# Kernel tuning notes

Measured on AMD Instinct MI355X. Metric: run time of the kernel, lower is better.

Reference implementation:

```python
import jax, jax.numpy as jnp
import numpy as np
import math

B, H, S, D = 4, 8, 2048, 64

def setup_inputs() -> dict:
    key = jax.random.key(0)
    k1, k2, k3, k4 = jax.random.split(key, 4)
    query = jax.random.normal(k1, (B, H, S, D), dtype=jnp.float32)
    key_t = jax.random.normal(k2, (B, H, S, D), dtype=jnp.float32)
    value = jax.random.normal(k3, (B, H, S, D), dtype=jnp.float32)
    mask = jax.random.randint(k4, (B, 1, S, S), 0, 2, dtype=jnp.int32)
    return {"query": query, "key": key_t, "value": value, "mask": mask}

def reference(query, key, value, mask):
    d = query.shape[-1]
    # Non-standard score: exp(QK^T) / sqrt(d), then masked fill, then softmax.
    logits = jnp.einsum('bhqd,bhkd->bhqk', query, key)
    scores = jnp.exp(logits) / math.sqrt(d)
    scores = jnp.where(mask == 0, jnp.float32(-1e9), scores)
    p_attn = jax.nn.softmax(scores, axis=-1)
    out = jnp.einsum('bhqk,bhkd->bhqd', p_attn, value)
    return out, p_attn
```

## Files before the change

kernel.cpp:

```cpp
#include <hip/hip_runtime.h>

#define NB 4
#define NH 8
#define NS 2048
#define ND 64
#define NBH (NB * NH)

typedef float f32x4  __attribute__((ext_vector_type(4)));
typedef float f32x16 __attribute__((ext_vector_type(16)));
typedef short s16x8  __attribute__((ext_vector_type(8)));
typedef unsigned int u32;

constexpr int TQ = 128;
constexpr int TK = 128;
constexpr int NT = NS / TK;

constexpr size_t PM_BYTES  = (size_t)NB * NS * (NS / 8);
constexpr size_t WSL_BYTES = 1 << 20;
constexpr size_t KHL_OFF   = PM_BYTES + WSL_BYTES;
constexpr size_t KHL_BYTES = (size_t)NBH * NT * 32768;
constexpr size_t QHI_OFF   = KHL_OFF + KHL_BYTES;
constexpr size_t QP_BYTES  = (size_t)NBH * NS * ND * 2;
constexpr size_t QLO_OFF   = QHI_OFF + QP_BYTES;
constexpr size_t REC_OFF   = QLO_OFF + QP_BYTES;
constexpr size_t REC4_BYTES= (size_t)NBH * NS * 4 * 16;
constexpr size_t REC2_BYTES= (size_t)NBH * NS * 2 * 16;
constexpr size_t WS_NEED4  = REC_OFF + REC4_BYTES;
constexpr size_t WS_NEED2  = REC_OFF + REC2_BYTES;

__device__ __forceinline__ u32 bf16_rne(u32 u) {
    return (u + 0x7FFFu + ((u >> 16) & 1u)) >> 16;
}
__device__ __forceinline__ void cvt_split(float x, u32 &hi, u32 &lo) {
    u32 h = bf16_rne(__float_as_uint(x));
    float hf = __uint_as_float(h << 16);
    lo = bf16_rne(__float_as_uint(x - hf));
    hi = h;
}

__global__ __launch_bounds__(256)
void prep_kernel(const int* __restrict__ mask, u32* __restrict__ pmT,
                 const float* __restrict__ K, short* __restrict__ khl,
                 const float* __restrict__ Q, short* __restrict__ qhi,
                 short* __restrict__ qlo, int* __restrict__ wsl)
{
    const int bid = blockIdx.x;
    if (bid == 0 && threadIdx.x == 0) wsl[0] = 0;

    if (bid < 2048) {
        int idx = bid * 256 + threadIdx.x;
        int ks = idx & 3;
        int q  = (idx >> 2) & 2047;
        int kt = (idx >> 13) & 15;
        int b  = idx >> 17;
        const int* mp = mask + ((size_t)b * NS + q) * NS + kt * 128 + ks * 32;
        u32 v = 0;
        #pragma unroll
        for (int i = 0; i < 8; ++i) {
            int4 a = *(const int4*)(mp + i * 4);
            v |= (u32)(a.x != 0) << (i * 4)
               | (u32)(a.y != 0) << (i * 4 + 1)
               | (u32)(a.z != 0) << (i * 4 + 2)
               | (u32)(a.w != 0) << (i * 4 + 3);
        }
        pmT[idx] = v;
    } else if (bid < 4096) {
        int idx = (bid - 2048) * 256 + threadIdx.x;
        int oct = idx & 7;
        int kg  = (idx >> 3) & 2047;
        int bh  = idx >> 14;
        const float* src = K + ((size_t)bh * NS + kg) * ND + oct * 8;
        f32x4 a = *(const f32x4*)src;
        f32x4 b = *(const f32x4*)(src + 4);
        u32 h[8], lo[8];
        cvt_split(a.x,h[0],lo[0]); cvt_split(a.y,h[1],lo[1]);
        cvt_split(a.z,h[2],lo[2]); cvt_split(a.w,h[3],lo[3]);
        cvt_split(b.x,h[4],lo[4]); cvt_split(b.y,h[5],lo[5]);
        cvt_split(b.z,h[6],lo[6]); cvt_split(b.w,h[7],lo[7]);
        union { u32 u[4]; s16x8 s; } H, L;
        #pragma unroll
        for (int e = 0; e < 4; ++e) {
            H.u[e] = h[2*e]  | (h[2*e+1]  << 16);
            L.u[e] = lo[2*e] | (lo[2*e+1] << 16);
        }
        int kt = kg >> 7, key = kg & 127, d_ = oct >> 1, hl = oct & 1;
        size_t base = (size_t)(bh * NT + kt) * 16384;
        size_t frag = (size_t)(((d_ * 2 + hl) * 128) + key) * 8;
        *(s16x8*)(khl + base + frag)        = H.s;
        *(s16x8*)(khl + base + 8192 + frag) = L.s;
    } else {
        int idx = (bid - 4096) * 256 + threadIdx.x;
        int oct = idx & 7;
        size_t row = (size_t)(idx >> 3);
        const float* src = Q + row * ND + oct * 8;
        f32x4 a = *(const f32x4*)src;
        f32x4 b = *(const f32x4*)(src + 4);
        u32 h[8], lo[8];
        cvt_split(a.x,h[0],lo[0]); cvt_split(a.y,h[1],lo[1]);
        cvt_split(a.z,h[2],lo[2]); cvt_split(a.w,h[3],lo[3]);
        cvt_split(b.x,h[4],lo[4]); cvt_split(b.y,h[5],lo[5]);
        cvt_split(b.z,h[6],lo[6]); cvt_split(b.w,h[7],lo[7]);
        union { u32 u[4]; s16x8 s; } H, L;
        #pragma unroll
        for (int e = 0; e < 4; ++e) {
            H.u[e] = h[2*e]  | (h[2*e+1]  << 16);
            L.u[e] = lo[2*e] | (lo[2*e+1] << 16);
        }
        *(s16x8*)(qhi + row * ND + oct * 8) = H.s;
        *(s16x8*)(qlo + row * ND + oct * 8) = L.s;
    }
}

template<int NZT>
__global__ __launch_bounds__(256, 4)
void qk6_kernel(const short* __restrict__ khl,
                const short* __restrict__ qhi,
                const short* __restrict__ qlo,
                const u32* __restrict__ pmT,
                float* __restrict__ p,
                float4* __restrict__ rec)
{
    const int t  = threadIdx.x;
    const int l  = t & 63;
    const int wv = t >> 6;
    const int hl = l >> 5;
    const int ln = l & 31;
    const int bh = blockIdx.x;
    const int b  = bh >> 3;
    const int q0 = blockIdx.y * TQ;
    const int z  = blockIdx.z;
    const int kt0 = z * (NT / NZT);
    constexpr int NIT = NT / NZT;
    constexpr int ZROWS = TQ / NZT;

    float* slab = p + ((size_t)bh * NS + q0 + z * ZROWS) * NS;
    constexpr int SLAB_F4_PER_IT = ZROWS * NS / 4 / NIT;
    const int q = q0 + wv * 32 + ln;

    s16x8 qh[4], ql[4];
    {
        const short* qr_h = qhi + ((size_t)bh * NS + q) * ND + hl * 8;
        const short* qr_l = qlo + ((size_t)bh * NS + q) * ND + hl * 8;
        #pragma unroll
        for (int d_ = 0; d_ < 4; ++d_) {
            qh[d_] = *(const s16x8*)(qr_h + d_ * 16);
            ql[d_] = *(const s16x8*)(qr_l + d_ * 16);
        }
    }

    const short* kh_head = khl + (size_t)(bh * NT) * 16384;
    const u32*   mrow    = pmT + (size_t)b * (NT * NS * 4) + (size_t)q * 4;

    uint4 mv = *(const uint4*)(mrow + (size_t)kt0 * (NS * 4));
    float m1 = -1e30f, m2 = -1e30f;
    int   i1 = 0;

    for (int kt = kt0, it = 0; it < NIT; ++kt, ++it) {
        {
            f32x4* base = (f32x4*)slab + (size_t)it * SLAB_F4_PER_IT + t;
            f32x4 z4 = {0.f, 0.f, 0.f, 0.f};
            #pragma unroll
            for (int i = 0; i < SLAB_F4_PER_IT / 256; ++i)
                __builtin_nontemporal_store(z4, base + i * 256);
        }

        uint4 mv_n = mv;
        if (it + 1 < NIT)
            mv_n = *(const uint4*)(mrow + (size_t)(kt + 1) * (NS * 4));

        const short* kb = kh_head + (size_t)kt * 16384;
        u32 mwv[4] = { mv.x >> (hl * 4), mv.y >> (hl * 4),
                       mv.z >> (hl * 4), mv.w >> (hl * 4) };

        auto top2 = [&](const f32x16& A, int ks) {
            u32 ws = mwv[ks];
            int kbase = kt * 128 + ks * 32 + hl * 4;
            #pragma unroll
            for (int r = 0; r < 16; ++r) {
                int bp = (r & 3) + 8 * (r >> 2);
                float v = ((ws >> bp) & 1u) ? A[r] : -1e30f;
                bool gt = v > m1;
                m2 = gt ? m1 : fmaxf(m2, v);
                m1 = fmaxf(m1, v);
                i1 = gt ? (kbase + bp) : i1;
            }
        };

        #pragma unroll
        for (int kp = 0; kp < 2; ++kp) {
            f32x16 acc0, acc1;
            #pragma unroll
            for (int r = 0; r < 16; ++r) { acc0[r] = 0.f; acc1[r] = 0.f; }
            #pragma unroll
            for (int d_ = 0; d_ < 4; ++d_) {
                const short* fr = kb + (size_t)((((d_ * 2 + hl) * 128) + kp * 64 + ln) * 8);
                s16x8 ah0 = *(const s16x8*)fr;
                s16x8 al0 = *(const s16x8*)(fr + 8192);
                s16x8 ah1 = *(const s16x8*)(fr + 256);
                s16x8 al1 = *(const s16x8*)(fr + 8192 + 256);
                acc0 = __builtin_amdgcn_mfma_f32_32x32x16_bf16(ah0, qh[d_], acc0, 0,0,0);
                acc1 = __builtin_amdgcn_mfma_f32_32x32x16_bf16(ah1, qh[d_], acc1, 0,0,0);
                acc0 = __builtin_amdgcn_mfma_f32_32x32x16_bf16(al0, qh[d_], acc0, 0,0,0);
                acc1 = __builtin_amdgcn_mfma_f32_32x32x16_bf16(al1, qh[d_], acc1, 0,0,0);
                acc0 = __builtin_amdgcn_mfma_f32_32x32x16_bf16(ah0, ql[d_], acc0, 0,0,0);
                acc1 = __builtin_amdgcn_mfma_f32_32x32x16_bf16(ah1, ql[d_], acc1, 0,0,0);
            }
            top2(acc0, kp * 2);
            top2(acc1, kp * 2 + 1);
        }

        mv = mv_n;
    }

    {
        float om1 = __shfl_xor(m1, 32, 64);
        float om2 = __shfl_xor(m2, 32, 64);
        int   oi1 = __shfl_xor(i1, 32, 64);
        float nm1, nm2; int ni1;
        if (om1 > m1)      { nm1 = om1; ni1 = oi1; nm2 = fmaxf(om2, m1); }
        else if (om1 < m1) { nm1 = m1;  ni1 = i1;  nm2 = fmaxf(m2, om1); }
        else { nm1 = m1; ni1 = i1; nm2 = (oi1 == i1) ? fmaxf(m2, om2) : m1; }
        m1 = nm1; i1 = ni1; m2 = nm2;
    }

    if (l < 32) {
        int row = bh * NS + q0 + wv * 32 + ln;
        rec[(size_t)row * NZT + z] = make_float4(m1, m2, __int_as_float(i1), 0.f);
    }
}

template<int NZT>
__global__ __launch_bounds__(256)
void finish_kernel(const float4* __restrict__ rec,
                   const float* __restrict__ V,
                   float* __restrict__ outp, float* __restrict__ p,
                   int* __restrict__ wsl, int wscap)
{
    int u = blockIdx.x * 256 + threadIdx.x;
    int row = u >> 4, c4 = u & 15;
    float4 r0 = rec[(size_t)row * NZT];
    float m1 = r0.x, m2 = r0.y;
    int   i1 = __float_as_int(r0.z);
    #pragma unroll
    for (int zz = 1; zz < NZT; ++zz) {
        float4 rz = rec[(size_t)row * NZT + zz];
        float a = rz.x;
        int   j = __float_as_int(rz.z);
        if (a > m1)      { m2 = fmaxf(rz.y, m1); m1 = a; i1 = j; }
        else if (a < m1) { m2 = fmaxf(m2, a); }
        else             { m2 = m1; }
    }

    float s1 = __expf(m1) * 0.125f;
    float s2 = __expf(m2) * 0.125f;
    bool clean = (m1 > -1e29f) && (s1 < 1e38f) && (s1 - s2 > 15.0f)
                 && (m1 - m2 > 1e-3f);
    int bh = row >> 11;
    if (clean) {
        const float* vr = V + ((size_t)bh * NS + i1) * ND;
        *(f32x4*)(outp + (size_t)row * ND + c4 * 4) = *(const f32x4*)(vr + c4 * 4);
        if (c4 == 0) p[(size_t)row * NS + i1] = 1.0f;
    } else if (c4 == 0 && wscap > 0) {
        int idx = atomicAdd(wsl, 1);
        if (idx < wscap) wsl[1 + idx] = row;
    }
}

__global__ __launch_bounds__(256)
void slow_rows_kernel(const float* __restrict__ Q, const float* __restrict__ K,
                      const float* __restrict__ V, const int* __restrict__ mask,
                      float* __restrict__ outp, float* __restrict__ p,
                      const int* __restrict__ wsl, int wscap, int allrows)
{
    __shared__ float qr[ND];
    __shared__ float redm[4], redz[4];
    __shared__ float ol[ND];
    int n;
    if (allrows) n = NBH * NS;
    else { n = wsl[0]; if (n > wscap) n = wscap; }
    const int t = threadIdx.x;
    const int lane = t & 63, w = t >> 6;

    for (int ii = blockIdx.x; ii < n; ii += gridDim.x) {
        int row = allrows ? ii : wsl[1 + ii];
        int bh = row >> 11, qq = row & (NS - 1), b = bh >> 3;
        const float* Qr = Q + (size_t)row * ND;
        const float* Kb = K + (size_t)bh * NS * ND;
        const float* Vb = V + (size_t)bh * NS * ND;
        const int*   mr = mask + (size_t)b * NS * NS + (size_t)qq * NS;

        __syncthreads();
        if (t < 16) ((float4*)qr)[t] = ((const float4*)Qr)[t];
        if (t < ND) ol[t] = 0.f;
        __syncthreads();

        float sc[8];
        int k0 = t * 8;
        #pragma unroll
        for (int i = 0; i < 8; ++i) {
            const float* kr = Kb + (size_t)(k0 + i) * ND;
            float a = 0.f;
            for (int d = 0; d < ND; d += 4) {
                float4 kv = *(const float4*)(kr + d);
                a += qr[d] * kv.x; a += qr[d + 1] * kv.y;
                a += qr[d + 2] * kv.z; a += qr[d + 3] * kv.w;
            }
            sc[i] = mr[k0 + i] ? __expf(a) * 0.125f : -1e9f;
        }
        float m = sc[0];
        #pragma unroll
        for (int i = 1; i < 8; ++i) m = fmaxf(m, sc[i]);
        #pragma unroll
        for (int d = 1; d < 64; d <<= 1) m = fmaxf(m, __shfl_xor(m, d, 64));
        if (lane == 0) redm[w] = m;
        __syncthreads();
        m = fmaxf(fmaxf(redm[0], redm[1]), fmaxf(redm[2], redm[3]));

        float e[8]; float z = 0.f;
        #pragma unroll
        for (int i = 0; i < 8; ++i) { e[i] = __expf(sc[i] - m); z += e[i]; }
        #pragma unroll
        for (int d = 1; d < 64; d <<= 1) z += __shfl_xor(z, d, 64);
        if (lane == 0) redz[w] = z;
        __syncthreads();
        float Z = redz[0] + redz[1] + redz[2] + redz[3];
        float inv = 1.f / Z;

        float* pr = p + (size_t)row * NS + k0;
        float4 o0, o1;
        o0.x = e[0] * inv; o0.y = e[1] * inv; o0.z = e[2] * inv; o0.w = e[3] * inv;
        o1.x = e[4] * inv; o1.y = e[5] * inv; o1.z = e[6] * inv; o1.w = e[7] * inv;
        *(float4*)pr = o0; *(float4*)(pr + 4) = o1;

        #pragma unroll
        for (int i = 0; i < 8; ++i) {
            float pv = e[i] * inv;
            if (pv > 0.f) {
                const float* vr = Vb + (size_t)(k0 + i) * ND;
                for (int d = 0; d < ND; ++d) atomicAdd(&ol[d], pv * vr[d]);
            }
        }
        __syncthreads();
        if (t < ND) outp[(size_t)row * ND + t] = ol[t];
    }
}

extern "C" void kernel_launch(void* const* d_in, const int* in_sizes, int n_in,
                              void* d_out, int out_size, void* d_ws, size_t ws_size,
                              hipStream_t stream)
{
    const float* Q    = (const float*)d_in[0];
    const float* K    = (const float*)d_in[1];
    const float* V    = (const float*)d_in[2];
    const int*   mask = (const int*)d_in[3];
    float* outp = (float*)d_out;
    float* p    = outp + (size_t)NBH * NS * ND;

    if (ws_size < WS_NEED2) {
        slow_rows_kernel<<<dim3(4096), 256, 0, stream>>>(Q, K, V, mask, outp, p,
                                                         nullptr, 0, 1);
        return;
    }

    u32* pmT   = (u32*)d_ws;
    int* wsl   = (int*)((char*)d_ws + PM_BYTES);
    int wscap  = (int)(WSL_BYTES / 4 - 1);
    short* khl = (short*)((char*)d_ws + KHL_OFF);
    short* qhi = (short*)((char*)d_ws + QHI_OFF);
    short* qlo = (short*)((char*)d_ws + QLO_OFF);
    float4* rec = (float4*)((char*)d_ws + REC_OFF);

    prep_kernel<<<dim3(6144), 256, 0, stream>>>(mask, pmT, K, khl, Q, qhi, qlo, wsl);

    if (ws_size >= WS_NEED4) {
        dim3 grid(NBH, NS / TQ, 4);
        qk6_kernel<4><<<grid, 256, 0, stream>>>(khl, qhi, qlo, pmT, p, rec);
        finish_kernel<4><<<dim3(NBH * NS * 16 / 256), 256, 0, stream>>>(
            rec, V, outp, p, wsl, wscap);
    } else {
        dim3 grid(NBH, NS / TQ, 2);
        qk6_kernel<2><<<grid, 256, 0, stream>>>(khl, qhi, qlo, pmT, p, rec);
        finish_kernel<2><<<dim3(NBH * NS * 16 / 256), 256, 0, stream>>>(
            rec, V, outp, p, wsl, wscap);
    }
    slow_rows_kernel<<<dim3(128), 256, 0, stream>>>(Q, K, V, mask, outp, p,
                                                    wsl, wscap, 0);
}
```

Measured before the change: 174.4 us.

## Split P zeroing into dedicated blocks within one kernel launch alongside QK blocks

Zeroing of the large p_attn output no longer happens inside the QK loop. It moves to 2048 dedicated blocks that are launched in the same grid as the compute blocks, which now have no zero stores interleaved. The key split also drops from 4 to 2 z-slices, and the launch_bounds occupancy hint of 4 is removed. The aim is to separate the write-bandwidth-bound zero fill from the compute so the two can overlap, at the cost of fewer compute blocks and possible scheduling imbalance.

```diff
diff --git a/kernel.cpp b/kernel.cpp
--- a/kernel.cpp
+++ b/kernel.cpp
@@ -14,6 +14,9 @@
 constexpr int TQ = 128;
 constexpr int TK = 128;
 constexpr int NT = NS / TK;
+constexpr int NZ = 2;
+constexpr int NZB = 2048;
+constexpr int NCB = NBH * (NS / TQ) * NZ;
 
 constexpr size_t PM_BYTES  = (size_t)NB * NS * (NS / 8);
 constexpr size_t WSL_BYTES = 1 << 20;
@@ -23,10 +26,8 @@
 constexpr size_t QP_BYTES  = (size_t)NBH * NS * ND * 2;
 constexpr size_t QLO_OFF   = QHI_OFF + QP_BYTES;
 constexpr size_t REC_OFF   = QLO_OFF + QP_BYTES;
-constexpr size_t REC4_BYTES= (size_t)NBH * NS * 4 * 16;
-constexpr size_t REC2_BYTES= (size_t)NBH * NS * 2 * 16;
-constexpr size_t WS_NEED4  = REC_OFF + REC4_BYTES;
-constexpr size_t WS_NEED2  = REC_OFF + REC2_BYTES;
+constexpr size_t REC_BYTES = (size_t)NBH * NS * NZ * 16;
+constexpr size_t WS_NEED   = REC_OFF + REC_BYTES;
 
 __device__ __forceinline__ u32 bf16_rne(u32 u) {
     return (u + 0x7FFFu + ((u >> 16) & 1u)) >> 16;
@@ -111,30 +112,38 @@
     }
 }
 
-template<int NZT>
-__global__ __launch_bounds__(256, 4)
-void qk6_kernel(const short* __restrict__ khl,
-                const short* __restrict__ qhi,
-                const short* __restrict__ qlo,
-                const u32* __restrict__ pmT,
-                float* __restrict__ p,
-                float4* __restrict__ rec)
-{
-    const int t  = threadIdx.x;
+__global__ __launch_bounds__(256)
+void mega_kernel(const short* __restrict__ khl,
+                 const short* __restrict__ qhi,
+                 const short* __restrict__ qlo,
+                 const u32* __restrict__ pmT,
+                 float* __restrict__ p,
+                 float4* __restrict__ rec)
+{
+    const int bid = blockIdx.x;
+    const int t   = threadIdx.x;
+
+    if (bid < NZB) {
+        f32x4* base = (f32x4*)p + (size_t)bid * 16384 + t;
+        f32x4 z4 = {0.f, 0.f, 0.f, 0.f};
+        #pragma unroll
+        for (int i = 0; i < 64; ++i)
+            __builtin_nontemporal_store(z4, base + i * 256);
+        return;
+    }
+
+    const int cb = bid - NZB;
+    const int bh = cb & 31;
+    const int qy = (cb >> 5) & 15;
+    const int z  = cb >> 9;
+    const int b  = bh >> 3;
+    const int q0 = qy * TQ;
+    const int kt0 = z * (NT / NZ);
+
     const int l  = t & 63;
     const int wv = t >> 6;
     const int hl = l >> 5;
     const int ln = l & 31;
-    const int bh = blockIdx.x;
-    const int b  = bh >> 3;
-    const int q0 = blockIdx.y * TQ;
-    const int z  = blockIdx.z;
-    const int kt0 = z * (NT / NZT);
-    constexpr int NIT = NT / NZT;
-    constexpr int ZROWS = TQ / NZT;
-
-    float* slab = p + ((size_t)bh * NS + q0 + z * ZROWS) * NS;
-    constexpr int SLAB_F4_PER_IT = ZROWS * NS / 4 / NIT;
     const int q = q0 + wv * 32 + ln;
 
     s16x8 qh[4], ql[4];
@@ -155,17 +164,9 @@
     float m1 = -1e30f, m2 = -1e30f;
     int   i1 = 0;
 
-    for (int kt = kt0, it = 0; it < NIT; ++kt, ++it) {
-        {
-            f32x4* base = (f32x4*)slab + (size_t)it * SLAB_F4_PER_IT + t;
-            f32x4 z4 = {0.f, 0.f, 0.f, 0.f};
-            #pragma unroll
-            for (int i = 0; i < SLAB_F4_PER_IT / 256; ++i)
-                __builtin_nontemporal_store(z4, base + i * 256);
-        }
-
+    for (int kt = kt0, it = 0; it < NT / NZ; ++kt, ++it) {
         uint4 mv_n = mv;
-        if (it + 1 < NIT)
+        if (it + 1 < NT / NZ)
             mv_n = *(const uint4*)(mrow + (size_t)(kt + 1) * (NS * 4));
 
         const short* kb = kh_head + (size_t)kt * 16384;
@@ -225,11 +226,10 @@
 
     if (l < 32) {
         int row = bh * NS + q0 + wv * 32 + ln;
-        rec[(size_t)row * NZT + z] = make_float4(m1, m2, __int_as_float(i1), 0.f);
-    }
-}
-
-template<int NZT>
+        rec[(size_t)row * NZ + z] = make_float4(m1, m2, __int_as_float(i1), 0.f);
+    }
+}
+
 __global__ __launch_bounds__(256)
 void finish_kernel(const float4* __restrict__ rec,
                    const float* __restrict__ V,
@@ -238,12 +238,12 @@
 {
     int u = blockIdx.x * 256 + threadIdx.x;
     int row = u >> 4, c4 = u & 15;
-    float4 r0 = rec[(size_t)row * NZT];
+    float4 r0 = rec[(size_t)row * NZ];
     float m1 = r0.x, m2 = r0.y;
     int   i1 = __float_as_int(r0.z);
     #pragma unroll
-    for (int zz = 1; zz < NZT; ++zz) {
-        float4 rz = rec[(size_t)row * NZT + zz];
+    for (int zz = 1; zz < NZ; ++zz) {
+        float4 rz = rec[(size_t)row * NZ + zz];
         float a = rz.x;
         int   j = __float_as_int(rz.z);
         if (a > m1)      { m2 = fmaxf(rz.y, m1); m1 = a; i1 = j; }
@@ -356,7 +356,7 @@
     float* outp = (float*)d_out;
     float* p    = outp + (size_t)NBH * NS * ND;
 
-    if (ws_size < WS_NEED2) {
+    if (ws_size < WS_NEED) {
         slow_rows_kernel<<<dim3(4096), 256, 0, stream>>>(Q, K, V, mask, outp, p,
                                                          nullptr, 0, 1);
         return;
@@ -372,17 +372,10 @@
 
     prep_kernel<<<dim3(6144), 256, 0, stream>>>(mask, pmT, K, khl, Q, qhi, qlo, wsl);
 
-    if (ws_size >= WS_NEED4) {
-        dim3 grid(NBH, NS / TQ, 4);
-        qk6_kernel<4><<<grid, 256, 0, stream>>>(khl, qhi, qlo, pmT, p, rec);
-        finish_kernel<4><<<dim3(NBH * NS * 16 / 256), 256, 0, stream>>>(
-            rec, V, outp, p, wsl, wscap);
-    } else {
-        dim3 grid(NBH, NS / TQ, 2);
-        qk6_kernel<2><<<grid, 256, 0, stream>>>(khl, qhi, qlo, pmT, p, rec);
-        finish_kernel<2><<<dim3(NBH * NS * 16 / 256), 256, 0, stream>>>(
-            rec, V, outp, p, wsl, wscap);
-    }
+    mega_kernel<<<dim3(NZB + NCB), 256, 0, stream>>>(khl, qhi, qlo, pmT, p, rec);
+
+    finish_kernel<<<dim3(NBH * NS * 16 / 256), 256, 0, stream>>>(rec, V, outp, p,
+                                                                 wsl, wscap);
     slow_rows_kernel<<<dim3(128), 256, 0, stream>>>(Q, K, V, mask, outp, p,
                                                     wsl, wscap, 0);
 }
```

Measured after the change: 224.4 us. 28.7% more time.
